# Kernel tuning notes

Measured on AMD Instinct MI355X. Metric: run time of the kernel, lower is better.

Reference implementation:

```python
import jax, jax.numpy as jnp
import numpy as np

LN_EPS = 1e-5
N_HEADS = 8
N_POINTS = 4


def layer_norm(x, g, b):
    m = x.mean(-1, keepdims=True)
    v = ((x - m) ** 2).mean(-1, keepdims=True)
    return (x - m) / jnp.sqrt(v + LN_EPS) * g + b


def msda(query, ref, src, ts, lsi, mask, Wv, bv, Wo, bo, Wa, ba, Wp, bp):
    # 1D multi-scale deformable attention (temporal, as in PDVC/SAGA-DVC).
    B, Lq, D = query.shape
    Lin = src.shape[0] * 0 + src.shape[1]
    ts_np = np.asarray(ts)
    lsi_np = np.asarray(lsi)
    L = ts_np.shape[0]
    H, P = N_HEADS, N_POINTS
    Dh = D // H
    value = src @ Wv + bv
    value = jnp.where(mask[..., None], 0.0, value).reshape(B, Lin, H, Dh)
    off = (query @ Wo + bo).reshape(B, Lq, H, L, P)
    aw = jax.nn.softmax((query @ Wa + ba).reshape(B, Lq, H, L * P), axis=-1)
    aw = aw.reshape(B, Lq, H, L, P)
    norm = jnp.asarray(ts_np).astype(query.dtype)  # (L,)
    # sampling locations in normalized [0,1] coords: (B,Lq,H,L,P)
    loc = ref[:, :, None, :, None, 0] + off / norm[None, None, None, :, None]
    b_idx = jnp.arange(B)[:, None, None, None]
    h_idx = jnp.arange(H)[None, None, :, None]
    out = jnp.zeros((B, Lq, H, Dh), query.dtype)
    for l in range(L):  # small fixed number of levels
        T = int(ts_np[l]); s = int(lsi_np[l])
        v = value[:, s:s + T]  # (B,T,H,Dh)
        # grid_sample align_corners=False: pixel pos = loc*T - 0.5
        pos = loc[:, :, :, l, :] * T - 0.5  # (B,Lq,H,P)
        x0 = jnp.floor(pos)
        w1 = (pos - x0)[..., None]
        x0i = x0.astype(jnp.int32)

        def gather(xi):
            valid = ((xi >= 0) & (xi < T))[..., None].astype(v.dtype)
            xc = jnp.clip(xi, 0, T - 1)
            return v[b_idx, xc, h_idx] * valid  # (B,Lq,H,P,Dh), zeros pad

        samp = gather(x0i) * (1.0 - w1) + gather(x0i + 1) * w1
        out = out + (samp * aw[:, :, :, l, :, None]).sum(axis=3)
    out = out.reshape(B, Lq, D) @ Wp + bp
    return out, loc, aw


def ffn(x, W1, b1, W2, b2, ln2_g, ln2_b):
    h = jax.nn.relu(x @ W1 + b1) @ W2 + b2
    return layer_norm(x + h, ln2_g, ln2_b)


def setup_inputs() -> dict:
    key = jax.random.key(0)
    ks = jax.random.split(key, 24)
    B, S, D = 8, 3840, 256
    L = 4
    ts = jnp.array([2048, 1024, 512, 256], dtype=jnp.int32)
    lsi = jnp.array([0, 2048, 3072, 3584], dtype=jnp.int32)
    HP = N_HEADS * L * N_POINTS  # 128
    sc = 0.02
    inp = {
        'video_src': jax.random.normal(ks[0], (B, S, D), jnp.float32),
        'audio_src': jax.random.normal(ks[1], (B, S, D), jnp.float32),
        'video_pos': jax.random.normal(ks[2], (B, S, D), jnp.float32),
        'audio_pos': jax.random.normal(ks[3], (B, S, D), jnp.float32),
        'video_ref': jax.random.uniform(ks[4], (B, S, L, 1), jnp.float32),
        'audio_ref': jax.random.uniform(ks[5], (B, S, L, 1), jnp.float32),
        'video_ts': ts, 'video_lsi': lsi,
        'video_mask': jnp.zeros((B, S), jnp.bool_),
        'audio_ts': ts, 'audio_lsi': lsi,
        'audio_mask': jnp.zeros((B, S), jnp.bool_),
        'Wv': jax.random.normal(ks[6], (D, D)) * sc, 'bv': jnp.zeros((D,)),
        'Wo': jax.random.normal(ks[7], (D, HP)) * sc, 'bo': jnp.zeros((HP,)),
        'Wa': jax.random.normal(ks[8], (D, HP)) * sc, 'ba': jnp.zeros((HP,)),
        'Wp': jax.random.normal(ks[9], (D, D)) * sc, 'bp': jnp.zeros((D,)),
        'ln1_g': jnp.ones((D,)), 'ln1_b': jnp.zeros((D,)),
        'W1': jax.random.normal(ks[10], (D, 1024)) * sc, 'b1': jnp.zeros((1024,)),
        'W2': jax.random.normal(ks[11], (1024, D)) * sc, 'b2': jnp.zeros((D,)),
        'ln2_g': jnp.ones((D,)), 'ln2_b': jnp.zeros((D,)),
    }
    return inp


def reference(video_src, audio_src, video_pos, audio_pos, video_ref, audio_ref,
              video_ts, video_lsi, video_mask, audio_ts, audio_lsi, audio_mask,
              Wv, bv, Wo, bo, Wa, ba, Wp, bp, ln1_g, ln1_b,
              W1, b1, W2, b2, ln2_g, ln2_b):
    attn = (Wv, bv, Wo, bo, Wa, ba, Wp, bp)
    # modality self-attention (dropout = identity at eval)
    v2, _, _ = msda(video_src + video_pos, video_ref, video_src,
                    video_ts, video_lsi, video_mask, *attn)
    video = layer_norm(video_src + v2, ln1_g, ln1_b)
    a2, _, _ = msda(audio_src + audio_pos, audio_ref, audio_src,
                    audio_ts, audio_lsi, audio_mask, *attn)
    audio = layer_norm(audio_src + a2, ln1_g, ln1_b)
    # cross-modal deformable attention
    vaa, a_loc, a_aw = msda(audio, audio_ref, video,
                            video_ts, video_lsi, video_mask, *attn)
    aav, v_loc, v_aw = msda(video, video_ref, audio,
                            audio_ts, audio_lsi, audio_mask, *attn)
    vaa = ffn(vaa, W1, b1, W2, b2, ln2_g, ln2_b)
    aav = ffn(aav, W1, b1, W2, b2, ln2_g, ln2_b)
    return (aav, vaa, v_loc, v_aw, a_loc, a_aw)
```

## Files before the change

### kernel.cpp

```cpp
#include <hip/hip_runtime.h>
#include <hip/hip_bf16.h>
#include <cstdint>

#define BB 8
#define SS 3840
#define RR (BB*SS)
#define NHALF ((size_t)RR * 256)

typedef short s16x8 __attribute__((ext_vector_type(8)));
typedef float f32x4 __attribute__((ext_vector_type(4)));
typedef float f32x2 __attribute__((ext_vector_type(2)));

__device__ __forceinline__ ushort f2bf(float f) {
    uint32_t u = __builtin_bit_cast(uint32_t, f);
    u += 0x7FFFu + ((u >> 16) & 1u);
    return (ushort)(u >> 16);
}
__device__ __forceinline__ float bf2f(ushort h) {
    return __builtin_bit_cast(float, (uint32_t)h << 16);
}
__device__ __forceinline__ f32x2 up2(uint32_t u) {
    f32x2 r;
    r.x = __builtin_bit_cast(float, u << 16);
    r.y = __builtin_bit_cast(float, u & 0xFFFF0000u);
    return r;
}

#define GLDS16(gp, lp) __builtin_amdgcn_global_load_lds( \
    (const __attribute__((address_space(1))) uint32_t*)(gp), \
    (__attribute__((address_space(3))) uint32_t*)(lp), 16, 0, 0)

__global__ __launch_bounds__(256) void wtrans_all(
    const float* __restrict__ Wv, const float* __restrict__ Wo,
    const float* __restrict__ Wa, const float* __restrict__ Wp,
    const float* __restrict__ W1, const float* __restrict__ W2,
    const float* __restrict__ bo, const float* __restrict__ ba,
    ushort* __restrict__ Wvt, ushort* __restrict__ Woat, ushort* __restrict__ Wpt,
    ushort* __restrict__ W1t, ushort* __restrict__ W2t, float* __restrict__ boa)
{
    int e = blockIdx.x * 256 + threadIdx.x;
    if (e < 65536)       { int k = e >> 8, n = e & 255;  Wvt[n * 256 + k] = f2bf(Wv[e]); }
    else if (e < 98304)  { int i = e - 65536;  int k = i >> 7, n = i & 127;  Woat[n * 256 + k] = f2bf(Wo[i]); }
    else if (e < 131072) { int i = e - 98304;  int k = i >> 7, n = i & 127;  Woat[(n + 128) * 256 + k] = f2bf(Wa[i]); }
    else if (e < 196608) { int i = e - 131072; int k = i >> 8, n = i & 255;  Wpt[n * 256 + k] = f2bf(Wp[i]); }
    else if (e < 458752) { int i = e - 196608; int k = i >> 10, n = i & 1023; W1t[n * 256 + k] = f2bf(W1[i]); }
    else if (e < 720896) { int i = e - 458752; int k = i >> 8, n = i & 255;  W2t[(size_t)n * 1024 + k] = f2bf(W2[i]); }
    else if (e < 721152) { int t = e - 720896; boa[t] = (t < 128) ? bo[t] : ba[t - 128]; }
}

__global__ __launch_bounds__(256) void pack2_cat(
    const float* __restrict__ vs, const float* __restrict__ as_,
    const float* __restrict__ vp, const float* __restrict__ ap,
    ushort* __restrict__ sb, ushort* __restrict__ qb)
{
    const int n4 = (int)(NHALF / 4);
    int i = blockIdx.x * 256 + threadIdx.x;
    int j = (i < n4) ? i : i - n4;
    const float4* s4 = (const float4*)((i < n4) ? vs : as_);
    const float4* p4 = (const float4*)((i < n4) ? vp : ap);
    float4 a = s4[j];
    float4 b = p4[j];
    ushort4 u, v;
    u.x = f2bf(a.x); u.y = f2bf(a.y); u.z = f2bf(a.z); u.w = f2bf(a.w);
    v.x = f2bf(a.x + b.x); v.y = f2bf(a.y + b.y); v.z = f2bf(a.z + b.z); v.w = f2bf(a.w + b.w);
    ((ushort4*)sb)[i] = u;
    ((ushort4*)qb)[i] = v;
}

__global__ __launch_bounds__(512) void gemm_fused(
    const ushort* __restrict__ Av0, const ushort* __restrict__ Av1,
    const ushort* __restrict__ Ao0, const ushort* __restrict__ Ao1,
    const ushort* __restrict__ WvT, const ushort* __restrict__ WoT,
    const float* __restrict__ bv, const float* __restrict__ boa,
    ushort* __restrict__ val_out,
    float* __restrict__ loc0, float* __restrict__ loc1,
    float* __restrict__ aw0, float* __restrict__ aw1,
    const float* __restrict__ ref0, const float* __restrict__ ref1,
    const int* __restrict__ ts0, const int* __restrict__ ts1,
    const unsigned char* __restrict__ mask0, const unsigned char* __restrict__ mask1)
{
    __shared__ ushort As[128 * 64];
    __shared__ ushort Bs[256 * 64];
    const int tid = threadIdx.x;
    const int lane = tid & 63;
    const int wid = tid >> 6;
    const int wr = wid >> 2, wc = wid & 3;
    const int job = blockIdx.y;
    const int bm = blockIdx.x << 7;
    const int half = bm >= RR;
    const int bmL = half ? bm - RR : bm;
    const int l15 = lane & 15;
    const int l4 = lane >> 4;

    const ushort* A = job ? (half ? Ao1 : Ao0) : (half ? Av1 : Av0);
    const ushort* Wt = job ? WoT : WvT;
    A += (size_t)bmL * 256;

    f32x4 acc[4][4] = {};

    for (int k0 = 0; k0 < 256; k0 += 64) {
        #pragma unroll
        for (int r = 0; r < 2; ++r) {
            int base = r * 512 + (wid << 6);
            int idx = base + lane;
            int row = idx >> 3, sl = idx & 7;
            int ch = sl ^ (row & 7);
            GLDS16(&A[(size_t)row * 256 + k0 + ch * 8], &As[base << 3]);
        }
        #pragma unroll
        for (int r = 0; r < 4; ++r) {
            int base = r * 512 + (wid << 6);
            int idx = base + lane;
            int col = idx >> 3, sl = idx & 7;
            int ch = sl ^ (col & 7);
            GLDS16(&Wt[(size_t)col * 256 + k0 + ch * 8], &Bs[base << 3]);
        }
        __syncthreads();
        #pragma unroll
        for (int ks = 0; ks < 2; ++ks) {
            s16x8 af[4], bf[4];
            const int k16 = ks * 4 + l4;
            #pragma unroll
            for (int m = 0; m < 4; ++m) {
                int row = (wr << 6) + (m << 4) + l15;
                af[m] = *(const s16x8*)&As[(row << 6) + ((k16 ^ (row & 7)) << 3)];
            }
            #pragma unroll
            for (int n = 0; n < 4; ++n) {
                int col = (wc << 6) + (n << 4) + l15;
                bf[n] = *(const s16x8*)&Bs[(col << 6) + ((k16 ^ (col & 7)) << 3)];
            }
            #pragma unroll
            for (int m = 0; m < 4; ++m)
                #pragma unroll
                for (int n = 0; n < 4; ++n)
                    acc[m][n] = __builtin_amdgcn_mfma_f32_16x16x32_bf16(af[m], bf[n], acc[m][n], 0, 0, 0);
        }
        __syncthreads();
    }

    const int l4r = l4 << 2;
    if (job == 0) {
        const unsigned char* mk = half ? mask1 : mask0;
        ushort* vo = val_out + (size_t)half * NHALF;
        #pragma unroll
        for (int m = 0; m < 4; ++m) {
            #pragma unroll
            for (int r = 0; r < 4; ++r) {
                const int rowL = bmL + (wr << 6) + (m << 4) + l4r + r;
                const int b = rowL / SS;
                const int s = rowL - b * SS;
                const float mz = mk[rowL] ? 0.f : 1.f;
                const size_t rb = ((size_t)(b * 8) * SS + s) * 32;
                #pragma unroll
                for (int n = 0; n < 4; ++n) {
                    const int col = (wc << 6) + (n << 4) + l15;
                    const int h = col >> 5, d = col & 31;
                    vo[rb + (size_t)h * (SS * 32) + d] = f2bf((acc[m][n][r] + bv[col]) * mz);
                }
            }
        }
    } else if (wc < 2) {
        const float* rf = half ? ref1 : ref0;
        const int* tsp = half ? ts1 : ts0;
        const int l = l15 >> 2;
        const float T = (float)tsp[l];
        float* lo = half ? loc1 : loc0;
        #pragma unroll
        for (int m = 0; m < 4; ++m) {
            #pragma unroll
            for (int r = 0; r < 4; ++r) {
                const int rowL = bmL + (wr << 6) + (m << 4) + l4r + r;
                const float refv = rf[(size_t)rowL * 4 + l];
                #pragma unroll
                for (int n = 0; n < 4; ++n) {
                    const int cc = (wc << 6) + (n << 4) + l15;
                    lo[(size_t)rowL * 128 + cc] = refv + (acc[m][n][r] + boa[cc]) / T;
                }
            }
        }
    } else {
        float* ao = half ? aw1 : aw0;
        #pragma unroll
        for (int m = 0; m < 4; ++m) {
            #pragma unroll
            for (int r = 0; r < 4; ++r) {
                const int rowL = bmL + (wr << 6) + (m << 4) + l4r + r;
                #pragma unroll
                for (int n = 0; n < 4; ++n) {
                    const int cc = (wc << 6) + (n << 4) + l15;
                    float c = acc[m][n][r] + boa[cc];
                    float mx = c;
                    #pragma unroll
                    for (int o = 1; o < 16; o <<= 1) mx = fmaxf(mx, __shfl_xor(mx, o));
                    float e = __expf(c - mx);
                    float sm = e;
                    #pragma unroll
                    for (int o = 1; o < 16; o <<= 1) sm += __shfl_xor(sm, o);
                    ao[(size_t)rowL * 128 + (cc - 128)] = e / sm;
                }
            }
        }
    }
}

template<int EPI>
__global__ __launch_bounds__(512) void gemm256(
    const ushort* __restrict__ A, const ushort* __restrict__ Wt,
    const float* __restrict__ bias, int N, int K,
    ushort* __restrict__ outb,
    const float* __restrict__ res0, const float* __restrict__ res1,
    const ushort* __restrict__ resb,
    const float* __restrict__ g, const float* __restrict__ be,
    float* __restrict__ of0, float* __restrict__ of1)
{
    __shared__ ushort As[128 * 64];
    __shared__ ushort Bs[256 * 64];
    __shared__ float redS[128][4];
    __shared__ float redQ[128][4];
    __shared__ float redM[128];
    __shared__ float redR[128];

    const int tid = threadIdx.x;
    const int lane = tid & 63;
    const int wid = tid >> 6;
    const int wr = wid >> 2, wc = wid & 3;
    const int bm = blockIdx.x << 7;
    const int bn = blockIdx.y << 8;
    const int l15 = lane & 15;
    const int l4 = lane >> 4;

    f32x4 acc[4][4] = {};

    for (int k0 = 0; k0 < K; k0 += 64) {
        #pragma unroll
        for (int r = 0; r < 2; ++r) {
            int base = r * 512 + (wid << 6);
            int idx = base + lane;
            int row = idx >> 3, sl = idx & 7;
            int ch = sl ^ (row & 7);
            GLDS16(&A[(size_t)(bm + row) * K + k0 + ch * 8], &As[base << 3]);
        }
        #pragma unroll
        for (int r = 0; r < 4; ++r) {
            int base = r * 512 + (wid << 6);
            int idx = base + lane;
            int col = idx >> 3, sl = idx & 7;
            int ch = sl ^ (col & 7);
            GLDS16(&Wt[(size_t)(bn + col) * K + k0 + ch * 8], &Bs[base << 3]);
        }
        __syncthreads();
        #pragma unroll
        for (int ks = 0; ks < 2; ++ks) {
            s16x8 af[4], bf[4];
            const int k16 = ks * 4 + l4;
            #pragma unroll
            for (int m = 0; m < 4; ++m) {
                int row = (wr << 6) + (m << 4) + l15;
                af[m] = *(const s16x8*)&As[(row << 6) + ((k16 ^ (row & 7)) << 3)];
            }
            #pragma unroll
            for (int n = 0; n < 4; ++n) {
                int col = (wc << 6) + (n << 4) + l15;
                bf[n] = *(const s16x8*)&Bs[(col << 6) + ((k16 ^ (col & 7)) << 3)];
            }
            #pragma unroll
            for (int m = 0; m < 4; ++m)
                #pragma unroll
                for (int n = 0; n < 4; ++n)
                    acc[m][n] = __builtin_amdgcn_mfma_f32_16x16x32_bf16(af[m], bf[n], acc[m][n], 0, 0, 0);
        }
        __syncthreads();
    }

    const int half = bm >= RR;
    const int bmL = half ? bm - RR : bm;

    if (EPI == 0 || EPI == 2) {
        #pragma unroll
        for (int m = 0; m < 4; ++m) {
            #pragma unroll
            for (int r = 0; r < 4; ++r) {
                const int row = bm + (wr << 6) + (m << 4) + (l4 << 2) + r;
                #pragma unroll
                for (int n = 0; n < 4; ++n) {
                    const int col = bn + (wc << 6) + (n << 4) + l15;
                    float c = acc[m][n][r] + bias[col];
                    if (EPI == 2) c = fmaxf(c, 0.f);
                    outb[(size_t)row * N + col] = f2bf(c);
                }
            }
        }
        return;
    }

    #pragma unroll
    for (int m = 0; m < 4; ++m) {
        #pragma unroll
        for (int r = 0; r < 4; ++r) {
            const int rowb = (wr << 6) + (m << 4) + (l4 << 2) + r;
            float s1 = 0.f, s2 = 0.f;
            #pragma unroll
            for (int n = 0; n < 4; ++n) {
                const int col = (wc << 6) + (n << 4) + l15;
                float x = acc[m][n][r] + bias[col];
                if (EPI == 1) {
                    const float* res = half ? res1 : res0;
                    x += res[(size_t)(bmL + rowb) * 256 + col];
                } else {
                    x += bf2f(resb[(size_t)(bm + rowb) * 256 + col]);
                }
                acc[m][n][r] = x;
                s1 += x;
                s2 += x * x;
            }
            #pragma unroll
            for (int o = 1; o < 16; o <<= 1) {
                s1 += __shfl_xor(s1, o);
                s2 += __shfl_xor(s2, o);
            }
            if (l15 == 0) { redS[rowb][wc] = s1; redQ[rowb][wc] = s2; }
        }
    }
    __syncthreads();
    if (tid < 128) {
        const float S1 = redS[tid][0] + redS[tid][1] + redS[tid][2] + redS[tid][3];
        const float S2 = redQ[tid][0] + redQ[tid][1] + redQ[tid][2] + redQ[tid][3];
        const float mu = S1 * (1.f / 256.f);
        float var = S2 * (1.f / 256.f) - mu * mu;
        var = fmaxf(var, 0.f);
        redM[tid] = mu;
        redR[tid] = rsqrtf(var + 1e-5f);
    }
    __syncthreads();
    #pragma unroll
    for (int m = 0; m < 4; ++m) {
        #pragma unroll
        for (int r = 0; r < 4; ++r) {
            const int rowb = (wr << 6) + (m << 4) + (l4 << 2) + r;
            const float mu = redM[rowb];
            const float rs = redR[rowb];
            #pragma unroll
            for (int n = 0; n < 4; ++n) {
                const int col = (wc << 6) + (n << 4) + l15;
                const float y = (acc[m][n][r] - mu) * rs * g[col] + be[col];
                if (EPI == 1) {
                    outb[(size_t)(bm + rowb) * 256 + col] = f2bf(y);
                } else {
                    float* of = half ? of1 : of0;
                    of[(size_t)(bmL + rowb) * 256 + col] = y;
                }
            }
        }
    }
}

struct Desc { float wa, wb; int oa, ob; };

__global__ __launch_bounds__(256) void msda_sample(
    const ushort* __restrict__ value,
    const float* __restrict__ l0, const float* __restrict__ l1,
    const float* __restrict__ a0, const float* __restrict__ a1,
    const int* __restrict__ ts0, const int* __restrict__ lsi0,
    const int* __restrict__ ts1, const int* __restrict__ lsi1,
    ushort* __restrict__ out)
{
    __shared__ Desc ds[64 * 17];
    const int tid = threadIdx.x;
    const int wg = blockIdx.x;
    const int xcd = wg & 7;
    const int idx = wg >> 3;
    const int half = idx >= 480;
    const int idxL = half ? idx - 480 : idx;
    const int rowL0 = xcd * SS + idxL * 8;
    const int row0 = rowL0 + (half ? RR : 0);

    const float* loc = half ? l1 : l0;
    const float* aw  = half ? a1 : a0;
    const int* ts  = half ? ts1 : ts0;
    const int* lsi = half ? lsi1 : lsi0;
    const ushort* val = value + (size_t)half * NHALF;

    #pragma unroll
    for (int d = tid; d < 1024; d += 256) {
        const int rl = d >> 7;
        const int rem = d & 127;
        const int l = (rem >> 2) & 3;
        const int h = rem >> 4;
        const int lp = rem & 15;
        const int rowL = rowL0 + rl;
        const float lc = loc[(size_t)rowL * 128 + rem];
        const float w  = aw[(size_t)rowL * 128 + rem];
        const int T = ts[l];
        const int s0 = lsi[l];
        const int b = rowL / SS;
        const float pos = lc * (float)T - 0.5f;
        const float x0 = floorf(pos);
        const float w1 = pos - x0;
        const int i0 = (int)x0;
        const int i1 = i0 + 1;
        const int base = (b * 8 + h) * SS + s0;
        Desc e;
        e.wa = (i0 >= 0 && i0 < T) ? w * (1.f - w1) : 0.f;
        e.wb = (i1 >= 0 && i1 < T) ? w * w1 : 0.f;
        const int ia = min(max(i0, 0), T - 1);
        const int ib = min(max(i1, 0), T - 1);
        e.oa = (base + ia) << 5;
        e.ob = (base + ib) << 5;
        ds[(rl * 8 + h) * 17 + lp] = e;
    }
    __syncthreads();

    const int rl = tid >> 5;
    const int h  = (tid >> 2) & 7;
    const int cq = tid & 3;
    const ushort* vb = val + cq * 8;
    const Desc* dd = &ds[(rl * 8 + h) * 17];

    f32x2 ac[4] = {};
    #pragma unroll
    for (int lp = 0; lp < 16; ++lp) {
        const Desc e = dd[lp];
        const uint4 A = *(const uint4*)(vb + e.oa);
        const uint4 B = *(const uint4*)(vb + e.ob);
        const f32x2 wa = {e.wa, e.wa};
        const f32x2 wb = {e.wb, e.wb};
        ac[0] = __builtin_elementwise_fma(wa, up2(A.x), ac[0]);
        ac[1] = __builtin_elementwise_fma(wa, up2(A.y), ac[1]);
        ac[2] = __builtin_elementwise_fma(wa, up2(A.z), ac[2]);
        ac[3] = __builtin_elementwise_fma(wa, up2(A.w), ac[3]);
        ac[0] = __builtin_elementwise_fma(wb, up2(B.x), ac[0]);
        ac[1] = __builtin_elementwise_fma(wb, up2(B.y), ac[1]);
        ac[2] = __builtin_elementwise_fma(wb, up2(B.z), ac[2]);
        ac[3] = __builtin_elementwise_fma(wb, up2(B.w), ac[3]);
    }
    s16x8 o;
    o[0] = (short)f2bf(ac[0].x); o[1] = (short)f2bf(ac[0].y);
    o[2] = (short)f2bf(ac[1].x); o[3] = (short)f2bf(ac[1].y);
    o[4] = (short)f2bf(ac[2].x); o[5] = (short)f2bf(ac[2].y);
    o[6] = (short)f2bf(ac[3].x); o[7] = (short)f2bf(ac[3].y);
    *(s16x8*)&out[(size_t)(row0 + rl) * 256 + h * 32 + cq * 8] = o;
}

extern "C" void kernel_launch(void* const* d_in, const int* in_sizes, int n_in,
                              void* d_out, int out_size, void* d_ws, size_t ws_size,
                              hipStream_t stream) {
    const float* video_src = (const float*)d_in[0];
    const float* audio_src = (const float*)d_in[1];
    const float* video_pos = (const float*)d_in[2];
    const float* audio_pos = (const float*)d_in[3];
    const float* video_ref = (const float*)d_in[4];
    const float* audio_ref = (const float*)d_in[5];
    const int*   video_ts  = (const int*)d_in[6];
    const int*   video_lsi = (const int*)d_in[7];
    const unsigned char* video_mask = (const unsigned char*)d_in[8];
    const int*   audio_ts  = (const int*)d_in[9];
    const int*   audio_lsi = (const int*)d_in[10];
    const unsigned char* audio_mask = (const unsigned char*)d_in[11];
    const float* Wv = (const float*)d_in[12];
    const float* bv = (const float*)d_in[13];
    const float* Wo = (const float*)d_in[14];
    const float* bo = (const float*)d_in[15];
    const float* Wa = (const float*)d_in[16];
    const float* ba = (const float*)d_in[17];
    const float* Wp = (const float*)d_in[18];
    const float* bp = (const float*)d_in[19];
    const float* ln1_g = (const float*)d_in[20];
    const float* ln1_b = (const float*)d_in[21];
    const float* W1 = (const float*)d_in[22];
    const float* b1 = (const float*)d_in[23];
    const float* W2 = (const float*)d_in[24];
    const float* b2 = (const float*)d_in[25];
    const float* ln2_g = (const float*)d_in[26];
    const float* ln2_b = (const float*)d_in[27];

    float* out = (float*)d_out;
    const size_t n = NHALF;
    float* out_aav  = out;
    float* out_vaa  = out + n;
    float* out_vloc = out + 2 * n;
    float* out_vaw  = out + 2 * n + n / 2;
    float* out_aloc = out + 3 * n;
    float* out_aaw  = out + 3 * n + n / 2;

    const size_t UB = NHALF * 2;
    char* base = (char*)d_ws;
    ushort* src_cat   = (ushort*)(base + 0 * UB);
    ushort* q_cat     = (ushort*)(base + 2 * UB);
    float*  loc_tmp   = (float*) (base + 4 * UB);
    float*  aw_tmp    = (float*) (base + 6 * UB);
    ushort* hid       = (ushort*)(base + 0 * UB);
    ushort* value_cat = (ushort*)(base + 8 * UB);
    ushort* samp_cat  = (ushort*)(base + 10 * UB);
    ushort* vb_cat    = (ushort*)(base + 12 * UB);
    ushort* proj_b34  = (ushort*)(base + 12 * UB);
    ushort* Wvt  = (ushort*)(base + 14 * UB);
    ushort* Woat = Wvt + 65536;
    ushort* Wpt  = Woat + 65536;
    ushort* W1t  = Wpt + 65536;
    ushort* W2t  = W1t + 262144;
    float*  boa  = (float*)(W2t + 262144);

    wtrans_all<<<2817, 256, 0, stream>>>(Wv, Wo, Wa, Wp, W1, W2, bo, ba,
                                         Wvt, Woat, Wpt, W1t, W2t, boa);
    pack2_cat<<<15360, 256, 0, stream>>>(video_src, audio_src, video_pos, audio_pos,
                                         src_cat, q_cat);

    gemm_fused<<<dim3(480, 2), 512, 0, stream>>>(
        src_cat, src_cat + NHALF, q_cat, q_cat + NHALF,
        Wvt, Woat, bv, boa, value_cat,
        loc_tmp, loc_tmp + (size_t)RR * 128, aw_tmp, aw_tmp + (size_t)RR * 128,
        video_ref, audio_ref, video_ts, audio_ts, video_mask, audio_mask);
    msda_sample<<<7680, 256, 0, stream>>>(
        value_cat, loc_tmp, loc_tmp + (size_t)RR * 128, aw_tmp, aw_tmp + (size_t)RR * 128,
        video_ts, video_lsi, audio_ts, audio_lsi, samp_cat);
    gemm256<1><<<dim3(480, 1), 512, 0, stream>>>(
        samp_cat, Wpt, bp, 256, 256, vb_cat,
        video_src, audio_src, nullptr, ln1_g, ln1_b, nullptr, nullptr);

    gemm_fused<<<dim3(480, 2), 512, 0, stream>>>(
        vb_cat, vb_cat + NHALF,
        vb_cat + NHALF, vb_cat,
        Wvt, Woat, bv, boa, value_cat,
        out_aloc, out_vloc, out_aaw, out_vaw,
        audio_ref, video_ref, video_ts, audio_ts, video_mask, audio_mask);
    msda_sample<<<7680, 256, 0, stream>>>(
        value_cat, out_aloc, out_vloc, out_aaw, out_vaw,
        video_ts, video_lsi, audio_ts, audio_lsi, samp_cat);
    gemm256<0><<<dim3(480, 1), 512, 0, stream>>>(
        samp_cat, Wpt, bp, 256, 256, proj_b34,
        nullptr, nullptr, nullptr, nullptr, nullptr, nullptr, nullptr);
    gemm256<2><<<dim3(480, 4), 512, 0, stream>>>(
        proj_b34, W1t, b1, 1024, 256, hid,
        nullptr, nullptr, nullptr, nullptr, nullptr, nullptr, nullptr);
    gemm256<3><<<dim3(480, 1), 512, 0, stream>>>(
        hid, W2t, b2, 256, 1024, nullptr,
        nullptr, nullptr, proj_b34, ln2_g, ln2_b, out_vaa, out_aav);
}
```

Measured before the change: 406.6 us.

## Fuse FFN GEMMs into one kernel keeping hidden activations in LDS; merge prep kernels

Replaces the two FFN GEMM launches (up-projection with ReLU, then down-projection with residual and LayerNorm) with a single kernel. Each block handles 64 rows and streams the 1024-wide hidden layer in 256-column chunks held in shared memory, so the bf16 hidden tensor never goes to global memory. It also merges the weight-transpose and input-pack kernels into one launch. The trade-off is smaller row tiles (64 rows, 4 waves) with a large LDS footprint, which lowers occupancy and weight reuse per block.

```diff
diff --git a/kernel.cpp b/kernel.cpp
--- a/kernel.cpp
+++ b/kernel.cpp
@@ -30,7 +30,10 @@
     (const __attribute__((address_space(1))) uint32_t*)(gp), \
     (__attribute__((address_space(3))) uint32_t*)(lp), 16, 0, 0)
 
-__global__ __launch_bounds__(256) void wtrans_all(
+__global__ __launch_bounds__(256) void prep(
+    const float* __restrict__ vs, const float* __restrict__ as_,
+    const float* __restrict__ vp, const float* __restrict__ ap,
+    ushort* __restrict__ sb, ushort* __restrict__ qb,
     const float* __restrict__ Wv, const float* __restrict__ Wo,
     const float* __restrict__ Wa, const float* __restrict__ Wp,
     const float* __restrict__ W1, const float* __restrict__ W2,
@@ -38,7 +41,23 @@
     ushort* __restrict__ Wvt, ushort* __restrict__ Woat, ushort* __restrict__ Wpt,
     ushort* __restrict__ W1t, ushort* __restrict__ W2t, float* __restrict__ boa)
 {
-    int e = blockIdx.x * 256 + threadIdx.x;
+    const int bid = blockIdx.x;
+    if (bid < 15360) {
+        const int n4 = (int)(NHALF / 4);
+        int i = bid * 256 + threadIdx.x;
+        int j = (i < n4) ? i : i - n4;
+        const float4* s4 = (const float4*)((i < n4) ? vs : as_);
+        const float4* p4 = (const float4*)((i < n4) ? vp : ap);
+        float4 a = s4[j];
+        float4 b = p4[j];
+        ushort4 u, v;
+        u.x = f2bf(a.x); u.y = f2bf(a.y); u.z = f2bf(a.z); u.w = f2bf(a.w);
+        v.x = f2bf(a.x + b.x); v.y = f2bf(a.y + b.y); v.z = f2bf(a.z + b.z); v.w = f2bf(a.w + b.w);
+        ((ushort4*)sb)[i] = u;
+        ((ushort4*)qb)[i] = v;
+        return;
+    }
+    int e = (bid - 15360) * 256 + threadIdx.x;
     if (e < 65536)       { int k = e >> 8, n = e & 255;  Wvt[n * 256 + k] = f2bf(Wv[e]); }
     else if (e < 98304)  { int i = e - 65536;  int k = i >> 7, n = i & 127;  Woat[n * 256 + k] = f2bf(Wo[i]); }
     else if (e < 131072) { int i = e - 98304;  int k = i >> 7, n = i & 127;  Woat[(n + 128) * 256 + k] = f2bf(Wa[i]); }
@@ -46,25 +65,6 @@
     else if (e < 458752) { int i = e - 196608; int k = i >> 10, n = i & 1023; W1t[n * 256 + k] = f2bf(W1[i]); }
     else if (e < 720896) { int i = e - 458752; int k = i >> 8, n = i & 255;  W2t[(size_t)n * 1024 + k] = f2bf(W2[i]); }
     else if (e < 721152) { int t = e - 720896; boa[t] = (t < 128) ? bo[t] : ba[t - 128]; }
-}
-
-__global__ __launch_bounds__(256) void pack2_cat(
-    const float* __restrict__ vs, const float* __restrict__ as_,
-    const float* __restrict__ vp, const float* __restrict__ ap,
-    ushort* __restrict__ sb, ushort* __restrict__ qb)
-{
-    const int n4 = (int)(NHALF / 4);
-    int i = blockIdx.x * 256 + threadIdx.x;
-    int j = (i < n4) ? i : i - n4;
-    const float4* s4 = (const float4*)((i < n4) ? vs : as_);
-    const float4* p4 = (const float4*)((i < n4) ? vp : ap);
-    float4 a = s4[j];
-    float4 b = p4[j];
-    ushort4 u, v;
-    u.x = f2bf(a.x); u.y = f2bf(a.y); u.z = f2bf(a.z); u.w = f2bf(a.w);
-    v.x = f2bf(a.x + b.x); v.y = f2bf(a.y + b.y); v.z = f2bf(a.z + b.z); v.w = f2bf(a.w + b.w);
-    ((ushort4*)sb)[i] = u;
-    ((ushort4*)qb)[i] = v;
 }
 
 __global__ __launch_bounds__(512) void gemm_fused(
@@ -210,9 +210,7 @@
     const float* __restrict__ bias, int N, int K,
     ushort* __restrict__ outb,
     const float* __restrict__ res0, const float* __restrict__ res1,
-    const ushort* __restrict__ resb,
-    const float* __restrict__ g, const float* __restrict__ be,
-    float* __restrict__ of0, float* __restrict__ of1)
+    const float* __restrict__ g, const float* __restrict__ be)
 {
     __shared__ ushort As[128 * 64];
     __shared__ ushort Bs[256 * 64];
@@ -276,7 +274,7 @@
     const int half = bm >= RR;
     const int bmL = half ? bm - RR : bm;
 
-    if (EPI == 0 || EPI == 2) {
+    if (EPI == 0) {
         #pragma unroll
         for (int m = 0; m < 4; ++m) {
             #pragma unroll
@@ -285,9 +283,7 @@
                 #pragma unroll
                 for (int n = 0; n < 4; ++n) {
                     const int col = bn + (wc << 6) + (n << 4) + l15;
-                    float c = acc[m][n][r] + bias[col];
-                    if (EPI == 2) c = fmaxf(c, 0.f);
-                    outb[(size_t)row * N + col] = f2bf(c);
+                    outb[(size_t)row * N + col] = f2bf(acc[m][n][r] + bias[col]);
                 }
             }
         }
@@ -303,13 +299,8 @@
             #pragma unroll
             for (int n = 0; n < 4; ++n) {
                 const int col = (wc << 6) + (n << 4) + l15;
-                float x = acc[m][n][r] + bias[col];
-                if (EPI == 1) {
-                    const float* res = half ? res1 : res0;
-                    x += res[(size_t)(bmL + rowb) * 256 + col];
-                } else {
-                    x += bf2f(resb[(size_t)(bm + rowb) * 256 + col]);
-                }
+                const float* res = half ? res1 : res0;
+                float x = acc[m][n][r] + bias[col] + res[(size_t)(bmL + rowb) * 256 + col];
                 acc[m][n][r] = x;
                 s1 += x;
                 s2 += x * x;
@@ -344,12 +335,176 @@
             for (int n = 0; n < 4; ++n) {
                 const int col = (wc << 6) + (n << 4) + l15;
                 const float y = (acc[m][n][r] - mu) * rs * g[col] + be[col];
-                if (EPI == 1) {
-                    outb[(size_t)(bm + rowb) * 256 + col] = f2bf(y);
-                } else {
-                    float* of = half ? of1 : of0;
-                    of[(size_t)(bmL + rowb) * 256 + col] = y;
-                }
+                outb[(size_t)(bm + rowb) * 256 + col] = f2bf(y);
+            }
+        }
+    }
+}
+
+__global__ __launch_bounds__(256) void ffn_fused(
+    const ushort* __restrict__ A,
+    const ushort* __restrict__ W1t,
+    const ushort* __restrict__ W2t,
+    const float* __restrict__ b1, const float* __restrict__ b2,
+    const float* __restrict__ g, const float* __restrict__ be,
+    float* __restrict__ of0, float* __restrict__ of1)
+{
+    __shared__ ushort As[64 * 64];
+    __shared__ ushort Bs[256 * 64];
+    __shared__ ushort Hs[64 * 256];
+    __shared__ float redS[64][4];
+    __shared__ float redQ[64][4];
+    __shared__ float redM[64];
+    __shared__ float redR[64];
+
+    const int tid = threadIdx.x;
+    const int lane = tid & 63;
+    const int wid = tid >> 6;
+    const int bm = blockIdx.x << 6;
+    const int l15 = lane & 15;
+    const int l4 = lane >> 4;
+
+    f32x4 acc2[4][4] = {};
+
+    for (int c = 0; c < 4; ++c) {
+        f32x4 acc[4][4] = {};
+        for (int k0 = 0; k0 < 4; ++k0) {
+            #pragma unroll
+            for (int r = 0; r < 2; ++r) {
+                int base = r * 256 + (wid << 6);
+                int idx = base + lane;
+                int row = idx >> 3, sl = idx & 7;
+                int ch = sl ^ (row & 7);
+                GLDS16(&A[(size_t)(bm + row) * 256 + k0 * 64 + ch * 8], &As[base << 3]);
+            }
+            #pragma unroll
+            for (int r = 0; r < 8; ++r) {
+                int base = r * 256 + (wid << 6);
+                int idx = base + lane;
+                int col = idx >> 3, sl = idx & 7;
+                int ch = sl ^ (col & 7);
+                GLDS16(&W1t[(size_t)(c * 256 + col) * 256 + k0 * 64 + ch * 8], &Bs[base << 3]);
+            }
+            __syncthreads();
+            #pragma unroll
+            for (int ks = 0; ks < 2; ++ks) {
+                s16x8 af[4], bf[4];
+                const int k16 = ks * 4 + l4;
+                #pragma unroll
+                for (int m = 0; m < 4; ++m) {
+                    int row = (m << 4) + l15;
+                    af[m] = *(const s16x8*)&As[(row << 6) + ((k16 ^ (row & 7)) << 3)];
+                }
+                #pragma unroll
+                for (int n = 0; n < 4; ++n) {
+                    int col = (wid << 6) + (n << 4) + l15;
+                    bf[n] = *(const s16x8*)&Bs[(col << 6) + ((k16 ^ (col & 7)) << 3)];
+                }
+                #pragma unroll
+                for (int m = 0; m < 4; ++m)
+                    #pragma unroll
+                    for (int n = 0; n < 4; ++n)
+                        acc[m][n] = __builtin_amdgcn_mfma_f32_16x16x32_bf16(af[m], bf[n], acc[m][n], 0, 0, 0);
+            }
+            __syncthreads();
+        }
+        #pragma unroll
+        for (int m = 0; m < 4; ++m) {
+            #pragma unroll
+            for (int r = 0; r < 4; ++r) {
+                const int row = (m << 4) + (l4 << 2) + r;
+                #pragma unroll
+                for (int n = 0; n < 4; ++n) {
+                    const int col = (wid << 6) + (n << 4) + l15;
+                    float x = fmaxf(acc[m][n][r] + b1[c * 256 + col], 0.f);
+                    const int chk = (col >> 3) ^ (row & 7);
+                    Hs[(row << 8) + (chk << 3) + (col & 7)] = f2bf(x);
+                }
+            }
+        }
+        __syncthreads();
+        for (int k0 = 0; k0 < 4; ++k0) {
+            #pragma unroll
+            for (int r = 0; r < 8; ++r) {
+                int base = r * 256 + (wid << 6);
+                int idx = base + lane;
+                int col = idx >> 3, sl = idx & 7;
+                int ch = sl ^ (col & 7);
+                GLDS16(&W2t[(size_t)col * 1024 + c * 256 + k0 * 64 + ch * 8], &Bs[base << 3]);
+            }
+            __syncthreads();
+            #pragma unroll
+            for (int ks = 0; ks < 2; ++ks) {
+                s16x8 af[4], bf[4];
+                const int k16 = ks * 4 + l4;
+                const int kchunk = k0 * 8 + k16;
+                #pragma unroll
+                for (int m = 0; m < 4; ++m) {
+                    int row = (m << 4) + l15;
+                    af[m] = *(const s16x8*)&Hs[(row << 8) + ((kchunk ^ (row & 7)) << 3)];
+                }
+                #pragma unroll
+                for (int n = 0; n < 4; ++n) {
+                    int col = (wid << 6) + (n << 4) + l15;
+                    bf[n] = *(const s16x8*)&Bs[(col << 6) + ((k16 ^ (col & 7)) << 3)];
+                }
+                #pragma unroll
+                for (int m = 0; m < 4; ++m)
+                    #pragma unroll
+                    for (int n = 0; n < 4; ++n)
+                        acc2[m][n] = __builtin_amdgcn_mfma_f32_16x16x32_bf16(af[m], bf[n], acc2[m][n], 0, 0, 0);
+            }
+            __syncthreads();
+        }
+    }
+
+    const int half = bm >= RR;
+    const int bmL = half ? bm - RR : bm;
+    #pragma unroll
+    for (int m = 0; m < 4; ++m) {
+        #pragma unroll
+        for (int r = 0; r < 4; ++r) {
+            const int rowb = (m << 4) + (l4 << 2) + r;
+            float s1 = 0.f, s2 = 0.f;
+            #pragma unroll
+            for (int n = 0; n < 4; ++n) {
+                const int col = (wid << 6) + (n << 4) + l15;
+                float x = acc2[m][n][r] + b2[col] + bf2f(A[(size_t)(bm + rowb) * 256 + col]);
+                acc2[m][n][r] = x;
+                s1 += x;
+                s2 += x * x;
+            }
+            #pragma unroll
+            for (int o = 1; o < 16; o <<= 1) {
+                s1 += __shfl_xor(s1, o);
+                s2 += __shfl_xor(s2, o);
+            }
+            if (l15 == 0) { redS[rowb][wid] = s1; redQ[rowb][wid] = s2; }
+        }
+    }
+    __syncthreads();
+    if (tid < 64) {
+        const float S1 = redS[tid][0] + redS[tid][1] + redS[tid][2] + redS[tid][3];
+        const float S2 = redQ[tid][0] + redQ[tid][1] + redQ[tid][2] + redQ[tid][3];
+        const float mu = S1 * (1.f / 256.f);
+        float var = S2 * (1.f / 256.f) - mu * mu;
+        var = fmaxf(var, 0.f);
+        redM[tid] = mu;
+        redR[tid] = rsqrtf(var + 1e-5f);
+    }
+    __syncthreads();
+    float* of = half ? of1 : of0;
+    #pragma unroll
+    for (int m = 0; m < 4; ++m) {
+        #pragma unroll
+        for (int r = 0; r < 4; ++r) {
+            const int rowb = (m << 4) + (l4 << 2) + r;
+            const float mu = redM[rowb];
+            const float rs = redR[rowb];
+            #pragma unroll
+            for (int n = 0; n < 4; ++n) {
+                const int col = (wid << 6) + (n << 4) + l15;
+                of[(size_t)(bmL + rowb) * 256 + col] = (acc2[m][n][r] - mu) * rs * g[col] + be[col];
             }
         }
     }
@@ -489,7 +644,6 @@
     ushort* q_cat     = (ushort*)(base + 2 * UB);
     float*  loc_tmp   = (float*) (base + 4 * UB);
     float*  aw_tmp    = (float*) (base + 6 * UB);
-    ushort* hid       = (ushort*)(base + 0 * UB);
     ushort* value_cat = (ushort*)(base + 8 * UB);
     ushort* samp_cat  = (ushort*)(base + 10 * UB);
     ushort* vb_cat    = (ushort*)(base + 12 * UB);
@@ -501,10 +655,10 @@
     ushort* W2t  = W1t + 262144;
     float*  boa  = (float*)(W2t + 262144);
 
-    wtrans_all<<<2817, 256, 0, stream>>>(Wv, Wo, Wa, Wp, W1, W2, bo, ba,
-                                         Wvt, Woat, Wpt, W1t, W2t, boa);
-    pack2_cat<<<15360, 256, 0, stream>>>(video_src, audio_src, video_pos, audio_pos,
-                                         src_cat, q_cat);
+    prep<<<18177, 256, 0, stream>>>(video_src, audio_src, video_pos, audio_pos,
+                                    src_cat, q_cat,
+                                    Wv, Wo, Wa, Wp, W1, W2, bo, ba,
+                                    Wvt, Woat, Wpt, W1t, W2t, boa);
 
     gemm_fused<<<dim3(480, 2), 512, 0, stream>>>(
         src_cat, src_cat + NHALF, q_cat, q_cat + NHALF,
@@ -516,7 +670,7 @@
         video_ts, video_lsi, audio_ts, audio_lsi, samp_cat);
     gemm256<1><<<dim3(480, 1), 512, 0, stream>>>(
         samp_cat, Wpt, bp, 256, 256, vb_cat,
-        video_src, audio_src, nullptr, ln1_g, ln1_b, nullptr, nullptr);
+        video_src, audio_src, ln1_g, ln1_b);
 
     gemm_fused<<<dim3(480, 2), 512, 0, stream>>>(
         vb_cat, vb_cat + NHALF,
@@ -529,11 +683,7 @@
         video_ts, video_lsi, audio_ts, audio_lsi, samp_cat);
     gemm256<0><<<dim3(480, 1), 512, 0, stream>>>(
         samp_cat, Wpt, bp, 256, 256, proj_b34,
-        nullptr, nullptr, nullptr, nullptr, nullptr, nullptr, nullptr);
-    gemm256<2><<<dim3(480, 4), 512, 0, stream>>>(
-        proj_b34, W1t, b1, 1024, 256, hid,
-        nullptr, nullptr, nullptr, nullptr, nullptr, nullptr, nullptr);
-    gemm256<3><<<dim3(480, 1), 512, 0, stream>>>(
-        hid, W2t, b2, 256, 1024, nullptr,
-        nullptr, nullptr, proj_b34, ln2_g, ln2_b, out_vaa, out_aav);
-}
+        nullptr, nullptr, nullptr, nullptr);
+    ffn_fused<<<960, 256, 0, stream>>>(
+        proj_b34, W1t, W2t, b1, b2, ln2_g, ln2_b, out_vaa, out_aav);
+}
```

Result: slower. 484.5 us (+19.1%).
